# Kernel tuning notes

Measured on AMD Instinct MI355X. Metric: run time of the kernel, lower is better.

Reference implementation:

```python
import jax, jax.numpy as jnp
import numpy as np

D_MODEL = 1024
N_HEADS = 16
HEAD_DIM = D_MODEL // N_HEADS


def setup_inputs() -> dict:
    key = jax.random.key(0)
    ks = jax.random.split(key, 5)
    B, T = 4, 2048
    x = jax.random.normal(ks[0], (B, T, D_MODEL), dtype=jnp.float32)
    s = 0.02
    W_qkv = jax.random.normal(ks[1], (D_MODEL, 3 * D_MODEL), dtype=jnp.float32) * s
    b_qkv = jnp.zeros((3 * D_MODEL,), dtype=jnp.float32)
    W_out = jax.random.normal(ks[2], (D_MODEL, D_MODEL), dtype=jnp.float32) * s
    b_out = jnp.zeros((D_MODEL,), dtype=jnp.float32)
    return {"x": x, "W_qkv": W_qkv, "b_qkv": b_qkv, "W_out": W_out, "b_out": b_out}


def reference(x, W_qkv, b_qkv, W_out, b_out):
    B, T, C = x.shape
    H, Dh = N_HEADS, HEAD_DIM
    qkv = x @ W_qkv + b_qkv                      # [B,T,3C]
    q, k, v = jnp.split(qkv, 3, axis=-1)
    q = q.reshape(B, T, H, Dh).transpose(0, 2, 1, 3)  # [B,H,T,Dh]
    k = k.reshape(B, T, H, Dh).transpose(0, 2, 1, 3)
    v = v.reshape(B, T, H, Dh).transpose(0, 2, 1, 3)
    scale = 1.0 / jnp.sqrt(jnp.float32(Dh))
    scores = jnp.einsum('bhqd,bhkd->bhqk', q, k) * scale  # [B,H,T,T]
    causal = jnp.tril(jnp.ones((T, T), dtype=bool))
    scores = jnp.where(causal[None, None], scores, jnp.float32(-jnp.inf))
    w = jax.nn.softmax(scores, axis=-1)
    y = jnp.einsum('bhqk,bhkd->bhqd', w, v)      # [B,H,T,Dh]
    y = y.transpose(0, 2, 1, 3).reshape(B, T, C)
    return y @ W_out + b_out
```

## Files before the change

kernel.cpp:

```cpp
#include <hip/hip_runtime.h>
#include <cstdint>
#include <math.h>

#define TT 2048
#define CC 1024
#define HH 16
#define DH 64
#define BB 4
#define MM 8192

typedef unsigned short u16;
typedef __bf16 bf16_t;
typedef bf16_t bf16x8 __attribute__((ext_vector_type(8)));
typedef float f32x4 __attribute__((ext_vector_type(4)));

static __device__ inline u16 f2bf(float f) {
    unsigned int u = __builtin_bit_cast(unsigned int, f);
    unsigned int lsb = (u >> 16) & 1u;
    u += 0x7fffu + lsb;
    return (u16)(u >> 16);
}

#define GLL16(gptr, lptr)                                                            \
    __builtin_amdgcn_global_load_lds(                                                \
        (__attribute__((address_space(1))) void*)(gptr),                             \
        (__attribute__((address_space(3))) void*)(lptr), 16, 0, 0)


__global__ void cast_x_kernel(const float* __restrict__ x, u16* __restrict__ xb, int n4) {
    int i = blockIdx.x * blockDim.x + threadIdx.x;
    if (i >= n4) return;
    float4 v = ((const float4*)x)[i];
    unsigned int p0 = (unsigned int)f2bf(v.x) | ((unsigned int)f2bf(v.y) << 16);
    unsigned int p1 = (unsigned int)f2bf(v.z) | ((unsigned int)f2bf(v.w) << 16);
    uint2 o; o.x = p0; o.y = p1;
    ((uint2*)xb)[i] = o;
}

__global__ void __launch_bounds__(256)
transpose_cast_kernel(const float* __restrict__ W, u16* __restrict__ Wt, int K, int N) {
    __shared__ u16 tile[32 * 34];
    const int tx = threadIdx.x & 31;
    const int ty = threadIdx.x >> 5;
    const int n0 = blockIdx.x * 32;
    const int k0 = blockIdx.y * 32;
#pragma unroll
    for (int i = 0; i < 4; ++i) {
        int k = ty + i * 8;
        tile[tx * 34 + k] = f2bf(W[(size_t)(k0 + k) * N + n0 + tx]);
    }
    __syncthreads();
    const int tx2 = threadIdx.x & 15;
    const int ty2 = threadIdx.x >> 4;
#pragma unroll
    for (int i = 0; i < 2; ++i) {
        int r = ty2 + i * 16;
        *(unsigned int*)&Wt[(size_t)(n0 + r) * K + k0 + 2 * tx2] =
            *(unsigned int*)&tile[r * 34 + 2 * tx2];
    }
}

template <int MODE>
__global__ void __launch_bounds__(256)
gemm_bt_kernel(const u16* __restrict__ A, const u16* __restrict__ Bt,
               const float* __restrict__ bias, float* __restrict__ Cout,
               u16* __restrict__ qws, u16* __restrict__ kws, u16* __restrict__ vtws,
               int Mdim, int Ndim, int Kdim) {
    __shared__ u16 As[2][128 * 32];
    __shared__ u16 Bs[2][128 * 32];

    const int tid  = threadIdx.x;
    const int w    = tid >> 6;
    const int lane = tid & 63;
    const int l15  = lane & 15;
    const int quad = lane >> 4;
    const int wm   = (w & 1) * 64;
    const int wn   = (w >> 1) * 64;
    const int m0   = blockIdx.y * 128;
    const int n0   = blockIdx.x * 128;

    const int row0  = tid >> 2;
    const int row1  = (tid + 256) >> 2;
    const int col8  = (tid & 3) << 3;

    f32x4 acc[4][4];
#pragma unroll
    for (int i = 0; i < 4; ++i)
#pragma unroll
        for (int j = 0; j < 4; ++j) acc[i][j] = (f32x4){0.f, 0.f, 0.f, 0.f};

    {
        if (MODE == 0) {
            int m = m0 + row0, b = m >> 11, t = m & 2047, h = col8 >> 6, d = col8 & 63;
            GLL16(&A[(((size_t)(b * HH + h) * TT + t) * DH) + d], &As[0][tid * 8]);
            m = m0 + row1; b = m >> 11; t = m & 2047;
            GLL16(&A[(((size_t)(b * HH + h) * TT + t) * DH) + d], &As[0][(tid + 256) * 8]);
        } else {
            GLL16(&A[(size_t)(m0 + row0) * Kdim + col8], &As[0][tid * 8]);
            GLL16(&A[(size_t)(m0 + row1) * Kdim + col8], &As[0][(tid + 256) * 8]);
        }
        GLL16(&Bt[(size_t)(n0 + row0) * Kdim + col8], &Bs[0][tid * 8]);
        GLL16(&Bt[(size_t)(n0 + row1) * Kdim + col8], &Bs[0][(tid + 256) * 8]);
    }

    const int nsteps = Kdim >> 5;
    for (int it = 0; it < nsteps; ++it) {
        const int buf = it & 1;
        __syncthreads();

        if (it + 1 < nsteps) {
            const int nbuf = buf ^ 1;
            const int kc = (it + 1) << 5;
            if (MODE == 0) {
                int kcc = kc + col8;
                int h = kcc >> 6, d = kcc & 63;
                int m = m0 + row0, b = m >> 11, t = m & 2047;
                GLL16(&A[(((size_t)(b * HH + h) * TT + t) * DH) + d], &As[nbuf][tid * 8]);
                m = m0 + row1; b = m >> 11; t = m & 2047;
                GLL16(&A[(((size_t)(b * HH + h) * TT + t) * DH) + d], &As[nbuf][(tid + 256) * 8]);
            } else {
                GLL16(&A[(size_t)(m0 + row0) * Kdim + kc + col8], &As[nbuf][tid * 8]);
                GLL16(&A[(size_t)(m0 + row1) * Kdim + kc + col8], &As[nbuf][(tid + 256) * 8]);
            }
            GLL16(&Bt[(size_t)(n0 + row0) * Kdim + kc + col8], &Bs[nbuf][tid * 8]);
            GLL16(&Bt[(size_t)(n0 + row1) * Kdim + kc + col8], &Bs[nbuf][(tid + 256) * 8]);
        }

        bf16x8 af[4], bfm[4];
#pragma unroll
        for (int mt = 0; mt < 4; ++mt)
            af[mt] = *(const bf16x8*)&As[buf][(wm + mt * 16 + l15) * 32 + quad * 8];
#pragma unroll
        for (int nt = 0; nt < 4; ++nt)
            bfm[nt] = *(const bf16x8*)&Bs[buf][(wn + nt * 16 + l15) * 32 + quad * 8];
#pragma unroll
        for (int mt = 0; mt < 4; ++mt)
#pragma unroll
            for (int nt = 0; nt < 4; ++nt)
                acc[mt][nt] = __builtin_amdgcn_mfma_f32_16x16x32_bf16(
                    af[mt], bfm[nt], acc[mt][nt], 0, 0, 0);
    }

#pragma unroll
    for (int mt = 0; mt < 4; ++mt) {
        int mrow_base = m0 + wm + mt * 16 + quad * 4;
#pragma unroll
        for (int nt = 0; nt < 4; ++nt) {
            int ncol = n0 + wn + nt * 16 + l15;
            float bv = bias[ncol];
            if (MODE == 0) {
#pragma unroll
                for (int r = 0; r < 4; ++r)
                    Cout[(size_t)(mrow_base + r) * Ndim + ncol] = acc[mt][nt][r] + bv;
            } else {
                int which = ncol >> 10, c = ncol & 1023;
                int h = c >> 6, d = c & 63;
                if (which == 2) {
                    int b = mrow_base >> 11, t = mrow_base & 2047;
                    int bh = b * HH + h;
                    ushort4 pv;
                    pv.x = f2bf(acc[mt][nt][0] + bv);
                    pv.y = f2bf(acc[mt][nt][1] + bv);
                    pv.z = f2bf(acc[mt][nt][2] + bv);
                    pv.w = f2bf(acc[mt][nt][3] + bv);
                    *(ushort4*)&vtws[((size_t)bh * DH + d) * TT + t] = pv;
                } else {
#pragma unroll
                    for (int r = 0; r < 4; ++r) {
                        int mrow = mrow_base + r;
                        int b = mrow >> 11, t = mrow & 2047;
                        int bh = b * HH + h;
                        float val = acc[mt][nt][r] + bv;
                        if (which == 0) {
                            qws[((size_t)bh * TT + t) * DH + d] = f2bf(val * 0.18033688f);
                        } else {
                            kws[((size_t)bh * TT + t) * DH + d] = f2bf(val);
                        }
                    }
                }
            }
        }
    }
}

__global__ void __launch_bounds__(512, 4)
attn_kernel(const u16* __restrict__ qws, const u16* __restrict__ kws,
            const u16* __restrict__ vtws, u16* __restrict__ yws) {
    __shared__ u16 Ks[64 * 68];
    __shared__ u16 Vs[64 * 68];
    __shared__ u16 Ps[8][16 * 68];

    const int tid  = threadIdx.x;
    const int w    = tid >> 6;
    const int lane = tid & 63;
    const int l15  = lane & 15;
    const int quad = lane >> 4;
    const int bh   = blockIdx.y;
    const int p    = blockIdx.x;

    const u16* Kbase = kws + (size_t)bh * TT * DH;
    const u16* Vbase = vtws + (size_t)bh * DH * TT;
    u16* Pw = &Ps[w][0];

    const int srow  = tid >> 3;
    const int scol8 = (tid & 7) << 3;

    bf16x8 aones;
#pragma unroll
    for (int i = 0; i < 8; ++i) aones[i] = __builtin_bit_cast(bf16_t, (u16)0x3F80);

#pragma unroll
    for (int phase = 0; phase < 2; ++phase) {
        const int qt   = phase == 0 ? (15 - p) : p;
        const int q0   = qt * 128;
        const int qr0  = q0 + w * 16;
        const int jend = q0 + 128;

        const u16* Qp = qws + ((size_t)bh * TT + qr0) * DH;
        bf16x8 bq[2];
#pragma unroll
        for (int kk = 0; kk < 2; ++kk)
            bq[kk] = *(const bf16x8*)&Qp[l15 * DH + kk * 32 + quad * 8];

        f32x4 o[4], ol;
#pragma unroll
        for (int dt = 0; dt < 4; ++dt) o[dt] = (f32x4){0.f, 0.f, 0.f, 0.f};
        ol = (f32x4){0.f, 0.f, 0.f, 0.f};

        uint4 pk = *(const uint4*)&Kbase[(size_t)srow * DH + scol8];
        uint4 pv = *(const uint4*)&Vbase[(size_t)srow * TT + scol8];

        for (int j0 = 0; j0 < jend; j0 += 64) {
            __syncthreads();
            *(uint4*)&Ks[srow * 68 + scol8] = pk;
            *(uint4*)&Vs[srow * 68 + scol8] = pv;
            __syncthreads();

            int jn = j0 + 64;
            if (jn < jend) {
                pk = *(const uint4*)&Kbase[(size_t)(jn + srow) * DH + scol8];
                pv = *(const uint4*)&Vbase[(size_t)srow * TT + jn + scol8];
            }

            if (j0 > qr0 + 15) continue;

            f32x4 s[4];
#pragma unroll
            for (int kt = 0; kt < 4; ++kt) s[kt] = (f32x4){0.f, 0.f, 0.f, 0.f};
#pragma unroll
            for (int kk = 0; kk < 2; ++kk)
#pragma unroll
                for (int kt = 0; kt < 4; ++kt) {
                    bf16x8 ak = *(const bf16x8*)&Ks[(kt * 16 + l15) * 68 + kk * 32 + quad * 8];
                    s[kt] = __builtin_amdgcn_mfma_f32_16x16x32_bf16(ak, bq[kk], s[kt], 0, 0, 0);
                }

            if (j0 + 63 > qr0) {
                int qy = qr0 + l15;
#pragma unroll
                for (int kt = 0; kt < 4; ++kt)
#pragma unroll
                    for (int r = 0; r < 4; ++r) {
                        int key = j0 + kt * 16 + quad * 4 + r;
                        if (key > qy) s[kt][r] = -INFINITY;
                    }
            }

#pragma unroll
            for (int kt = 0; kt < 4; ++kt)
#pragma unroll
                for (int r = 0; r < 4; ++r)
                    s[kt][r] = __builtin_amdgcn_exp2f(s[kt][r]);

#pragma unroll
            for (int kt = 0; kt < 4; ++kt) {
                ushort4 pkd;
                pkd.x = f2bf(s[kt][0]);
                pkd.y = f2bf(s[kt][1]);
                pkd.z = f2bf(s[kt][2]);
                pkd.w = f2bf(s[kt][3]);
                *(ushort4*)&Pw[l15 * 68 + kt * 16 + quad * 4] = pkd;
            }
            asm volatile("s_waitcnt lgkmcnt(0)" ::: "memory");

#pragma unroll
            for (int kk = 0; kk < 2; ++kk) {
                bf16x8 bp = *(const bf16x8*)&Pw[l15 * 68 + kk * 32 + quad * 8];
#pragma unroll
                for (int dt = 0; dt < 4; ++dt) {
                    bf16x8 av = *(const bf16x8*)&Vs[(dt * 16 + l15) * 68 + kk * 32 + quad * 8];
                    o[dt] = __builtin_amdgcn_mfma_f32_16x16x32_bf16(av, bp, o[dt], 0, 0, 0);
                }
                ol = __builtin_amdgcn_mfma_f32_16x16x32_bf16(aones, bp, ol, 0, 0, 0);
            }
        }

        float rinv = 1.f / ol[0];
        int t = qr0 + l15;
#pragma unroll
        for (int dt = 0; dt < 4; ++dt) {
            ushort4 yv;
            yv.x = f2bf(o[dt][0] * rinv);
            yv.y = f2bf(o[dt][1] * rinv);
            yv.z = f2bf(o[dt][2] * rinv);
            yv.w = f2bf(o[dt][3] * rinv);
            *(ushort4*)&yws[((size_t)bh * TT + t) * DH + dt * 16 + quad * 4] = yv;
        }
    }
}


extern "C" void kernel_launch(void* const* d_in, const int* in_sizes, int n_in,
                              void* d_out, int out_size, void* d_ws, size_t ws_size,
                              hipStream_t stream) {
    const float* x     = (const float*)d_in[0];
    const float* W_qkv = (const float*)d_in[1];
    const float* b_qkv = (const float*)d_in[2];
    const float* W_out = (const float*)d_in[3];
    const float* b_out = (const float*)d_in[4];
    float* out = (float*)d_out;

    char* ws = (char*)d_ws;
    u16* xb   = (u16*)ws; ws += (size_t)MM * CC * 2;
    u16* wqt  = (u16*)ws; ws += (size_t)3 * CC * CC * 2;
    u16* wot  = (u16*)ws; ws += (size_t)CC * CC * 2;
    u16* qws  = (u16*)ws; ws += (size_t)MM * CC * 2;
    u16* kws  = (u16*)ws; ws += (size_t)MM * CC * 2;
    u16* vtws = (u16*)ws; ws += (size_t)MM * CC * 2;
    u16* yws  = (u16*)ws; ws += (size_t)MM * CC * 2;

    cast_x_kernel<<<(MM * CC / 4) / 256, 256, 0, stream>>>(x, xb, MM * CC / 4);
    transpose_cast_kernel<<<dim3(3 * CC / 32, CC / 32), 256, 0, stream>>>(W_qkv, wqt, CC, 3 * CC);
    transpose_cast_kernel<<<dim3(CC / 32, CC / 32), 256, 0, stream>>>(W_out, wot, CC, CC);

    gemm_bt_kernel<1><<<dim3(24, 64), 256, 0, stream>>>(
        xb, wqt, b_qkv, nullptr, qws, kws, vtws, MM, 3 * CC, CC);

    attn_kernel<<<dim3(8, BB * HH), 512, 0, stream>>>(qws, kws, vtws, yws);

    gemm_bt_kernel<0><<<dim3(8, 64), 256, 0, stream>>>(
        yws, wot, b_out, out, nullptr, nullptr, nullptr, MM, CC, CC);
}
```

Measured before the change: 278.6 us.

## Fuse fp32-to-bf16 cast of x into QKV GEMM A-tile loading

Removes the separate cast kernel for x and has the QKV GEMM read fp32 x directly into registers, convert it to bf16 and write the result to LDS, with a one-step register prefetch. This avoids writing and re-reading a bf16 copy of x and saves one launch. In exchange, the GEMM now reads twice the A bytes per tile and does conversion ALU work that the async global-to-LDS path used to avoid. The attention grid is also transposed so that consecutive blocks cover different heads instead of different query tiles, which changes the block scheduling order.

```diff
diff --git a/kernel.cpp b/kernel.cpp
--- a/kernel.cpp
+++ b/kernel.cpp
@@ -21,21 +21,14 @@
     return (u16)(u >> 16);
 }
 
+static __device__ inline unsigned int pack2(float a, float b) {
+    return (unsigned int)f2bf(a) | ((unsigned int)f2bf(b) << 16);
+}
+
 #define GLL16(gptr, lptr)                                                            \
     __builtin_amdgcn_global_load_lds(                                                \
         (__attribute__((address_space(1))) void*)(gptr),                             \
         (__attribute__((address_space(3))) void*)(lptr), 16, 0, 0)
-
-
-__global__ void cast_x_kernel(const float* __restrict__ x, u16* __restrict__ xb, int n4) {
-    int i = blockIdx.x * blockDim.x + threadIdx.x;
-    if (i >= n4) return;
-    float4 v = ((const float4*)x)[i];
-    unsigned int p0 = (unsigned int)f2bf(v.x) | ((unsigned int)f2bf(v.y) << 16);
-    unsigned int p1 = (unsigned int)f2bf(v.z) | ((unsigned int)f2bf(v.w) << 16);
-    uint2 o; o.x = p0; o.y = p1;
-    ((uint2*)xb)[i] = o;
-}
 
 __global__ void __launch_bounds__(256)
 transpose_cast_kernel(const float* __restrict__ W, u16* __restrict__ Wt, int K, int N) {
@@ -62,7 +55,7 @@
 
 template <int MODE>
 __global__ void __launch_bounds__(256)
-gemm_bt_kernel(const u16* __restrict__ A, const u16* __restrict__ Bt,
+gemm_bt_kernel(const void* __restrict__ Araw, const u16* __restrict__ Bt,
                const float* __restrict__ bias, float* __restrict__ Cout,
                u16* __restrict__ qws, u16* __restrict__ kws, u16* __restrict__ vtws,
                int Mdim, int Ndim, int Kdim) {
@@ -79,9 +72,12 @@
     const int m0   = blockIdx.y * 128;
     const int n0   = blockIdx.x * 128;
 
-    const int row0  = tid >> 2;
-    const int row1  = (tid + 256) >> 2;
-    const int col8  = (tid & 3) << 3;
+    const int row0 = tid >> 2;
+    const int row1 = row0 + 64;
+    const int col8 = (tid & 3) << 3;
+
+    const float* Ax = (const float*)Araw;
+    const u16*   Ay = (const u16*)Araw;
 
     f32x4 acc[4][4];
 #pragma unroll
@@ -89,21 +85,44 @@
 #pragma unroll
         for (int j = 0; j < 4; ++j) acc[i][j] = (f32x4){0.f, 0.f, 0.f, 0.f};
 
-    {
-        if (MODE == 0) {
-            int m = m0 + row0, b = m >> 11, t = m & 2047, h = col8 >> 6, d = col8 & 63;
-            GLL16(&A[(((size_t)(b * HH + h) * TT + t) * DH) + d], &As[0][tid * 8]);
-            m = m0 + row1; b = m >> 11; t = m & 2047;
-            GLL16(&A[(((size_t)(b * HH + h) * TT + t) * DH) + d], &As[0][(tid + 256) * 8]);
-        } else {
-            GLL16(&A[(size_t)(m0 + row0) * Kdim + col8], &As[0][tid * 8]);
-            GLL16(&A[(size_t)(m0 + row1) * Kdim + col8], &As[0][(tid + 256) * 8]);
-        }
-        GLL16(&Bt[(size_t)(n0 + row0) * Kdim + col8], &Bs[0][tid * 8]);
-        GLL16(&Bt[(size_t)(n0 + row1) * Kdim + col8], &Bs[0][(tid + 256) * 8]);
-    }
+    float4 a0lo, a0hi, a1lo, a1hi;
+    auto loadA = [&](int kc) {
+        const float* p0 = &Ax[(size_t)(m0 + row0) * Kdim + kc + col8];
+        a0lo = *(const float4*)p0;
+        a0hi = *(const float4*)(p0 + 4);
+        const float* p1 = &Ax[(size_t)(m0 + row1) * Kdim + kc + col8];
+        a1lo = *(const float4*)p1;
+        a1hi = *(const float4*)(p1 + 4);
+    };
+    auto writeA = [&](int buf) {
+        uint4 u0, u1;
+        u0.x = pack2(a0lo.x, a0lo.y); u0.y = pack2(a0lo.z, a0lo.w);
+        u0.z = pack2(a0hi.x, a0hi.y); u0.w = pack2(a0hi.z, a0hi.w);
+        u1.x = pack2(a1lo.x, a1lo.y); u1.y = pack2(a1lo.z, a1lo.w);
+        u1.z = pack2(a1hi.x, a1hi.y); u1.w = pack2(a1hi.z, a1hi.w);
+        *(uint4*)&As[buf][tid * 8]         = u0;
+        *(uint4*)&As[buf][(tid + 256) * 8] = u1;
+    };
+    auto stageA_gll = [&](int buf, int kc) {
+        int m = m0 + row0, b = m >> 11, t = m & 2047;
+        int kcc = kc + col8, h = kcc >> 6, d = kcc & 63;
+        GLL16(&Ay[(((size_t)(b * HH + h) * TT + t) * DH) + d], &As[buf][tid * 8]);
+        m = m0 + row1; b = m >> 11; t = m & 2047;
+        GLL16(&Ay[(((size_t)(b * HH + h) * TT + t) * DH) + d], &As[buf][(tid + 256) * 8]);
+    };
 
     const int nsteps = Kdim >> 5;
+
+    if (MODE == 1) {
+        loadA(0);
+        writeA(0);
+        loadA(32);
+    } else {
+        stageA_gll(0, 0);
+    }
+    GLL16(&Bt[(size_t)(n0 + row0) * Kdim + col8], &Bs[0][tid * 8]);
+    GLL16(&Bt[(size_t)(n0 + row1) * Kdim + col8], &Bs[0][(tid + 256) * 8]);
+
     for (int it = 0; it < nsteps; ++it) {
         const int buf = it & 1;
         __syncthreads();
@@ -111,16 +130,11 @@
         if (it + 1 < nsteps) {
             const int nbuf = buf ^ 1;
             const int kc = (it + 1) << 5;
-            if (MODE == 0) {
-                int kcc = kc + col8;
-                int h = kcc >> 6, d = kcc & 63;
-                int m = m0 + row0, b = m >> 11, t = m & 2047;
-                GLL16(&A[(((size_t)(b * HH + h) * TT + t) * DH) + d], &As[nbuf][tid * 8]);
-                m = m0 + row1; b = m >> 11; t = m & 2047;
-                GLL16(&A[(((size_t)(b * HH + h) * TT + t) * DH) + d], &As[nbuf][(tid + 256) * 8]);
+            if (MODE == 1) {
+                writeA(nbuf);
+                if (it + 2 < nsteps) loadA((it + 2) << 5);
             } else {
-                GLL16(&A[(size_t)(m0 + row0) * Kdim + kc + col8], &As[nbuf][tid * 8]);
-                GLL16(&A[(size_t)(m0 + row1) * Kdim + kc + col8], &As[nbuf][(tid + 256) * 8]);
+                stageA_gll(nbuf, kc);
             }
             GLL16(&Bt[(size_t)(n0 + row0) * Kdim + kc + col8], &Bs[nbuf][tid * 8]);
             GLL16(&Bt[(size_t)(n0 + row1) * Kdim + kc + col8], &Bs[nbuf][(tid + 256) * 8]);
@@ -195,8 +209,8 @@
     const int lane = tid & 63;
     const int l15  = lane & 15;
     const int quad = lane >> 4;
-    const int bh   = blockIdx.y;
-    const int p    = blockIdx.x;
+    const int bh   = blockIdx.x;
+    const int p    = blockIdx.y;
 
     const u16* Kbase = kws + (size_t)bh * TT * DH;
     const u16* Vbase = vtws + (size_t)bh * DH * TT;
@@ -321,7 +335,6 @@
     float* out = (float*)d_out;
 
     char* ws = (char*)d_ws;
-    u16* xb   = (u16*)ws; ws += (size_t)MM * CC * 2;
     u16* wqt  = (u16*)ws; ws += (size_t)3 * CC * CC * 2;
     u16* wot  = (u16*)ws; ws += (size_t)CC * CC * 2;
     u16* qws  = (u16*)ws; ws += (size_t)MM * CC * 2;
@@ -329,14 +342,13 @@
     u16* vtws = (u16*)ws; ws += (size_t)MM * CC * 2;
     u16* yws  = (u16*)ws; ws += (size_t)MM * CC * 2;
 
-    cast_x_kernel<<<(MM * CC / 4) / 256, 256, 0, stream>>>(x, xb, MM * CC / 4);
     transpose_cast_kernel<<<dim3(3 * CC / 32, CC / 32), 256, 0, stream>>>(W_qkv, wqt, CC, 3 * CC);
     transpose_cast_kernel<<<dim3(CC / 32, CC / 32), 256, 0, stream>>>(W_out, wot, CC, CC);
 
     gemm_bt_kernel<1><<<dim3(24, 64), 256, 0, stream>>>(
-        xb, wqt, b_qkv, nullptr, qws, kws, vtws, MM, 3 * CC, CC);
-
-    attn_kernel<<<dim3(8, BB * HH), 512, 0, stream>>>(qws, kws, vtws, yws);
+        x, wqt, b_qkv, nullptr, qws, kws, vtws, MM, 3 * CC, CC);
+
+    attn_kernel<<<dim3(BB * HH, 8), 512, 0, stream>>>(qws, kws, vtws, yws);
 
     gemm_bt_kernel<0><<<dim3(8, 64), 256, 0, stream>>>(
         yws, wot, b_out, out, nullptr, nullptr, nullptr, MM, CC, CC);
```

Result: slower. 310.4 us (+11.4%).
